# Kernel tuning notes

Measured on AMD Instinct MI355X. Metric: run time of the kernel, lower is better.

## Reference

```python
import jax, jax.numpy as jnp
import numpy as np

N, D, NUM_CLASSES = 8192, 256, 64
MARGIN_SAME = 0.9
MARGIN_DIFF = 0.5


def setup_inputs() -> dict:
    key = jax.random.key(0)
    k1, k2 = jax.random.split(key)
    inputs = jax.random.normal(k1, (N, D), dtype=jnp.float32)
    # contrastive losses with cosine-style margins expect unit-norm embeddings
    inputs = inputs / jnp.linalg.norm(inputs, axis=1, keepdims=True)
    targets = jax.random.randint(k2, (N,), 0, NUM_CLASSES, dtype=jnp.int64)
    return {"inputs": inputs, "targets": targets}


def reference(inputs, targets):
    n = inputs.shape[0]
    sim = jnp.matmul(inputs, inputs.T)  # [n, n] pairwise similarities

    same = targets[:, None] == targets[None, :]  # [n, n]
    pos_mask = same & (sim < 1.0)                # pos_pair_ selection per row
    neg_mask = ~same                             # neg_pair_ selection per row

    pos_active = pos_mask & (sim < MARGIN_SAME)  # contribute 1 - sim
    neg_active = neg_mask & (sim > MARGIN_DIFF)  # contribute sim

    # sum over all rows, divided by n (sort in the original is irrelevant to sums)
    loss = (jnp.sum(jnp.where(pos_active, 1.0 - sim, 0.0))
            + jnp.sum(jnp.where(neg_active, sim, 0.0))) / n

    prec = jnp.float32(0.0)  # original: c is never incremented

    # original reports means of the LAST row's pos_pair_ / neg_pair_
    last_sim = sim[n - 1]
    lp = pos_mask[n - 1]
    ln = neg_mask[n - 1]
    mean_pos_sim = jnp.sum(jnp.where(lp, last_sim, 0.0)) / jnp.maximum(
        jnp.sum(lp).astype(jnp.float32), 1.0)
    mean_neg_sim = jnp.sum(jnp.where(ln, last_sim, 0.0)) / jnp.maximum(
        jnp.sum(ln).astype(jnp.float32), 1.0)

    return (loss, prec, mean_pos_sim, mean_neg_sim)
```

## Files before the change

### kernel.cpp

```cpp
#include <hip/hip_runtime.h>
#include <hip/hip_bf16.h>

#define N_ 8192
#define D_ 256
#define BM 128
#define BK 32
#define NB (N_ / BM)
#define NT (NB * (NB + 1) / 2)
#define KSTEPS (D_ / BK)

typedef __bf16 bf16x8 __attribute__((ext_vector_type(8)));
typedef float f32x4 __attribute__((ext_vector_type(4)));

__global__ void cvt_kernel(const float4* __restrict__ in, ushort4* __restrict__ out, int n4,
                           double* __restrict__ accd) {
  int i = blockIdx.x * blockDim.x + threadIdx.x;
  if (blockIdx.x == 0 && threadIdx.x < 128) accd[threadIdx.x] = 0.0;
  if (i >= n4) return;
  float4 v = in[i];
  union { __hip_bfloat16 h[4]; ushort4 u; } t;
  t.h[0] = __float2bfloat16(v.x);
  t.h[1] = __float2bfloat16(v.y);
  t.h[2] = __float2bfloat16(v.z);
  t.h[3] = __float2bfloat16(v.w);
  out[i] = t.u;
}

__global__ __launch_bounds__(256, 4) void simloss_kernel(
    const __hip_bfloat16* __restrict__ Xb, const int* __restrict__ tg,
    double* __restrict__ accd) {
  __shared__ __align__(16) char lds[32768];

  const int t = blockIdx.x;
  int bi = (int)(((2.0f * NB + 1.0f) -
                  sqrtf((2.0f * NB + 1.0f) * (2.0f * NB + 1.0f) - 8.0f * (float)t)) * 0.5f);
  if (bi < 0) bi = 0;
  if (bi > NB - 1) bi = NB - 1;
  while (((bi + 1) * NB - ((bi + 1) * bi) / 2) <= t) ++bi;
  while ((bi * NB - (bi * (bi - 1)) / 2) > t) --bi;
  const int bj = bi + (t - (bi * NB - (bi * (bi - 1)) / 2));

  const int tid = threadIdx.x;
  const int lane = tid & 63, wv = tid >> 6;
  const int wr = wv >> 1, wc = wv & 1;
  const int rowA0 = bi * BM, rowB0 = bj * BM;

  const int c0 = (wv * 2 + 0) * 64 + lane;
  const int c1 = (wv * 2 + 1) * 64 + lane;
  const int r0 = c0 >> 2, s0 = (c0 & 3) ^ ((r0 >> 1) & 3);
  const int r1 = c1 >> 2, s1 = (c1 & 3) ^ ((r1 >> 1) & 3);
  const __hip_bfloat16* gA0 = Xb + (size_t)(rowA0 + r0) * D_ + s0 * 8;
  const __hip_bfloat16* gA1 = Xb + (size_t)(rowA0 + r1) * D_ + s1 * 8;
  const __hip_bfloat16* gB0 = Xb + (size_t)(rowB0 + r0) * D_ + s0 * 8;
  const __hip_bfloat16* gB1 = Xb + (size_t)(rowB0 + r1) * D_ + s1 * 8;
  char* lA0 = lds + c0 * 16;
  char* lA1 = lds + c1 * 16;
  char* lB0 = lds + 16384 + c0 * 16;
  char* lB1 = lds + 16384 + c1 * 16;

#define GLDS(g, l) \
  __builtin_amdgcn_global_load_lds((const __attribute__((address_space(1))) void*)(g), \
                                   (__attribute__((address_space(3))) void*)(l), 16, 0, 0)
#define STAGE(buf, kt)                       \
  do {                                       \
    GLDS(gA0 + (kt) * BK, lA0 + (buf) * 8192); \
    GLDS(gA1 + (kt) * BK, lA1 + (buf) * 8192); \
    GLDS(gB0 + (kt) * BK, lB0 + (buf) * 8192); \
    GLDS(gB1 + (kt) * BK, lB1 + (buf) * 8192); \
  } while (0)

  const int fr = lane & 15, sl = lane >> 4;
  const int rswz = sl ^ ((fr >> 1) & 3);
  const int aoff = (wr * 64 + fr) * 64 + rswz * 16;
  const int boff = (wc * 64 + fr) * 64 + rswz * 16;

  f32x4 acc[4][4] = {};

  STAGE(0, 0);
  __syncthreads();
#pragma unroll
  for (int kt = 0; kt < KSTEPS; ++kt) {
    const int cur = kt & 1;
    if (kt < KSTEPS - 1) STAGE(cur ^ 1, kt + 1);
    const char* Ab = lds + cur * 8192;
    const char* Bb = lds + 16384 + cur * 8192;
    bf16x8 af[4], bfr[4];
#pragma unroll
    for (int m = 0; m < 4; ++m) af[m] = *(const bf16x8*)(Ab + aoff + m * 1024);
#pragma unroll
    for (int n = 0; n < 4; ++n) bfr[n] = *(const bf16x8*)(Bb + boff + n * 1024);
#pragma unroll
    for (int m = 0; m < 4; ++m)
#pragma unroll
      for (int n = 0; n < 4; ++n)
        acc[m][n] = __builtin_amdgcn_mfma_f32_16x16x32_bf16(af[m], bfr[n], acc[m][n], 0, 0, 0);
    __syncthreads();
  }
#undef STAGE
#undef GLDS

  const int cRow = (lane >> 4) * 4, cCol = lane & 15;
  int tj[4], ti[4][4];
#pragma unroll
  for (int n = 0; n < 4; ++n) tj[n] = tg[rowB0 + wc * 64 + n * 16 + cCol];
#pragma unroll
  for (int m = 0; m < 4; ++m)
#pragma unroll
    for (int r = 0; r < 4; ++r) ti[m][r] = tg[rowA0 + wr * 64 + m * 16 + cRow + r];

  float pc = 0.f, ps = 0.f, ns = 0.f;
#pragma unroll
  for (int m = 0; m < 4; ++m)
#pragma unroll
    for (int n = 0; n < 4; ++n)
#pragma unroll
      for (int r = 0; r < 4; ++r) {
        float s = acc[m][n][r];
        bool same = (ti[m][r] == tj[n]);
        if (same & (s < 0.9f)) { pc += 1.0f; ps += s; }
        if ((!same) & (s > 0.5f)) { ns += s; }
      }

  if (bj == NB - 1 && wc == 1 && cCol == 15) {
    const int tlast = tj[3];
    float lps = 0.f, lns = 0.f, lpc = 0.f, lnc = 0.f;
#pragma unroll
    for (int m = 0; m < 4; ++m)
#pragma unroll
      for (int r = 0; r < 4; ++r) {
        float s = acc[m][3][r];
        bool same = (ti[m][r] == tlast);
        if (same && s < 1.0f) { lps += s; lpc += 1.f; }
        if (!same) { lns += s; lnc += 1.f; }
      }
    atomicAdd(&accd[96], (double)lps);
    atomicAdd(&accd[97], (double)lpc);
    atomicAdd(&accd[98], (double)lns);
    atomicAdd(&accd[99], (double)lnc);
  }

#pragma unroll
  for (int off = 32; off > 0; off >>= 1) {
    pc += __shfl_down(pc, off);
    ps += __shfl_down(ps, off);
    ns += __shfl_down(ns, off);
  }
  float* red = (float*)lds;
  if (lane == 0) { red[0 * 4 + wv] = pc; red[1 * 4 + wv] = ps; red[2 * 4 + wv] = ns; }
  __syncthreads();
  if (tid == 0) {
    double w = (bi == bj) ? 1.0 : 2.0;
    double* slot = accd + (blockIdx.x & 31) * 3;
    atomicAdd(&slot[0], w * (double)(red[0] + red[1] + red[2] + red[3]));
    atomicAdd(&slot[1], w * (double)(red[4] + red[5] + red[6] + red[7]));
    atomicAdd(&slot[2], w * (double)(red[8] + red[9] + red[10] + red[11]));
  }
}

__global__ void finalize_kernel(const double* __restrict__ accd, float* __restrict__ out) {
  double pc = 0.0, ps = 0.0, ns = 0.0;
#pragma unroll
  for (int i = 0; i < 32; ++i) {
    pc += accd[i * 3 + 0];
    ps += accd[i * 3 + 1];
    ns += accd[i * 3 + 2];
  }
  double loss = (pc - ps + ns) / (double)N_;
  out[0] = (float)loss;
  out[1] = 0.0f;
  out[2] = (float)(accd[96] / fmax(accd[97], 1.0));
  out[3] = (float)(accd[98] / fmax(accd[99], 1.0));
}

extern "C" void kernel_launch(void* const* d_in, const int* in_sizes, int n_in,
                              void* d_out, int out_size, void* d_ws, size_t ws_size,
                              hipStream_t stream) {
  const float* X = (const float*)d_in[0];
  const int* tg = (const int*)d_in[1];
  float* out = (float*)d_out;
  double* accd = (double*)d_ws;
  __hip_bfloat16* Xb = (__hip_bfloat16*)((char*)d_ws + 1024);

  int n4 = N_ * D_ / 4;
  cvt_kernel<<<(n4 + 255) / 256, 256, 0, stream>>>((const float4*)X, (ushort4*)Xb, n4, accd);

  simloss_kernel<<<NT, 256, 0, stream>>>(Xb, tg, accd);

  finalize_kernel<<<1, 1, 0, stream>>>(accd, out);
}
```

Before: 49.76 us.

## Load MFMA operands directly from global memory instead of LDS staging

Drops the double-buffered global-to-LDS staging and its per-step barriers. Each lane now reads its bf16x8 MFMA fragments straight from global memory, depending on L1/L2 cache for reuse across waves. This removes LDS traffic and synchronisation and frees LDS for occupancy, but it duplicates global loads across waves and loses the explicit prefetch overlap.

```diff
diff --git a/kernel.cpp b/kernel.cpp
--- a/kernel.cpp
+++ b/kernel.cpp
@@ -4,10 +4,9 @@
 #define N_ 8192
 #define D_ 256
 #define BM 128
-#define BK 32
 #define NB (N_ / BM)
 #define NT (NB * (NB + 1) / 2)
-#define KSTEPS (D_ / BK)
+#define KSTEPS (D_ / 32)
 
 typedef __bf16 bf16x8 __attribute__((ext_vector_type(8)));
 typedef float f32x4 __attribute__((ext_vector_type(4)));
@@ -29,8 +28,6 @@
 __global__ __launch_bounds__(256, 4) void simloss_kernel(
     const __hip_bfloat16* __restrict__ Xb, const int* __restrict__ tg,
     double* __restrict__ accd) {
-  __shared__ __align__(16) char lds[32768];
-
   const int t = blockIdx.x;
   int bi = (int)(((2.0f * NB + 1.0f) -
                   sqrtf((2.0f * NB + 1.0f) * (2.0f * NB + 1.0f) - 8.0f * (float)t)) * 0.5f);
@@ -45,61 +42,33 @@
   const int wr = wv >> 1, wc = wv & 1;
   const int rowA0 = bi * BM, rowB0 = bj * BM;
 
-  const int c0 = (wv * 2 + 0) * 64 + lane;
-  const int c1 = (wv * 2 + 1) * 64 + lane;
-  const int r0 = c0 >> 2, s0 = (c0 & 3) ^ ((r0 >> 1) & 3);
-  const int r1 = c1 >> 2, s1 = (c1 & 3) ^ ((r1 >> 1) & 3);
-  const __hip_bfloat16* gA0 = Xb + (size_t)(rowA0 + r0) * D_ + s0 * 8;
-  const __hip_bfloat16* gA1 = Xb + (size_t)(rowA0 + r1) * D_ + s1 * 8;
-  const __hip_bfloat16* gB0 = Xb + (size_t)(rowB0 + r0) * D_ + s0 * 8;
-  const __hip_bfloat16* gB1 = Xb + (size_t)(rowB0 + r1) * D_ + s1 * 8;
-  char* lA0 = lds + c0 * 16;
-  char* lA1 = lds + c1 * 16;
-  char* lB0 = lds + 16384 + c0 * 16;
-  char* lB1 = lds + 16384 + c1 * 16;
-
-#define GLDS(g, l) \
-  __builtin_amdgcn_global_load_lds((const __attribute__((address_space(1))) void*)(g), \
-                                   (__attribute__((address_space(3))) void*)(l), 16, 0, 0)
-#define STAGE(buf, kt)                       \
-  do {                                       \
-    GLDS(gA0 + (kt) * BK, lA0 + (buf) * 8192); \
-    GLDS(gA1 + (kt) * BK, lA1 + (buf) * 8192); \
-    GLDS(gB0 + (kt) * BK, lB0 + (buf) * 8192); \
-    GLDS(gB1 + (kt) * BK, lB1 + (buf) * 8192); \
-  } while (0)
-
   const int fr = lane & 15, sl = lane >> 4;
-  const int rswz = sl ^ ((fr >> 1) & 3);
-  const int aoff = (wr * 64 + fr) * 64 + rswz * 16;
-  const int boff = (wc * 64 + fr) * 64 + rswz * 16;
+  const __hip_bfloat16* pA[4];
+  const __hip_bfloat16* pB[4];
+#pragma unroll
+  for (int m = 0; m < 4; ++m)
+    pA[m] = Xb + (size_t)(rowA0 + wr * 64 + m * 16 + fr) * D_ + sl * 8;
+#pragma unroll
+  for (int n = 0; n < 4; ++n)
+    pB[n] = Xb + (size_t)(rowB0 + wc * 64 + n * 16 + fr) * D_ + sl * 8;
 
   f32x4 acc[4][4] = {};
 
-  STAGE(0, 0);
-  __syncthreads();
 #pragma unroll
   for (int kt = 0; kt < KSTEPS; ++kt) {
-    const int cur = kt & 1;
-    if (kt < KSTEPS - 1) STAGE(cur ^ 1, kt + 1);
-    const char* Ab = lds + cur * 8192;
-    const char* Bb = lds + 16384 + cur * 8192;
     bf16x8 af[4], bfr[4];
 #pragma unroll
-    for (int m = 0; m < 4; ++m) af[m] = *(const bf16x8*)(Ab + aoff + m * 1024);
+    for (int m = 0; m < 4; ++m) af[m] = *(const bf16x8*)(pA[m] + kt * 32);
 #pragma unroll
-    for (int n = 0; n < 4; ++n) bfr[n] = *(const bf16x8*)(Bb + boff + n * 1024);
+    for (int n = 0; n < 4; ++n) bfr[n] = *(const bf16x8*)(pB[n] + kt * 32);
 #pragma unroll
     for (int m = 0; m < 4; ++m)
 #pragma unroll
       for (int n = 0; n < 4; ++n)
         acc[m][n] = __builtin_amdgcn_mfma_f32_16x16x32_bf16(af[m], bfr[n], acc[m][n], 0, 0, 0);
-    __syncthreads();
   }
-#undef STAGE
-#undef GLDS
 
-  const int cRow = (lane >> 4) * 4, cCol = lane & 15;
+  const int cRow = sl * 4, cCol = fr;
   int tj[4], ti[4][4];
 #pragma unroll
   for (int n = 0; n < 4; ++n) tj[n] = tg[rowB0 + wc * 64 + n * 16 + cCol];
@@ -145,8 +114,8 @@
     ps += __shfl_down(ps, off);
     ns += __shfl_down(ns, off);
   }
-  float* red = (float*)lds;
-  if (lane == 0) { red[0 * 4 + wv] = pc; red[1 * 4 + wv] = ps; red[2 * 4 + wv] = ns; }
+  __shared__ float red[12];
+  if (lane == 0) { red[0 + wv] = pc; red[4 + wv] = ps; red[8 + wv] = ns; }
   __syncthreads();
   if (tid == 0) {
     double w = (bi == bj) ? 1.0 : 2.0;
```

Measured after the change: 93.21 us. +87.3%, slower.

## Triple-buffer LDS with explicit vmcnt waits and remap tile order

Applied to the files above, without the earlier changes.

Replaces the double-buffered K loop with a three-stage ring buffer. Loads for steps 0-2 are issued up front, and explicit s_waitcnt vmcnt counts plus raw barriers allow two global->LDS stages to stay in flight while MFMAs run. The block index is also permuted with a stride so neighbouring blocks map to tiles spread across the triangle, which likely changes L2 locality. Launch bounds drop to 3 blocks/CU to make room for the 48KB of LDS, trading occupancy for deeper prefetch. Correctness depends on the hand-counted vmcnt values matching the issued loads.

```diff
diff --git a/kernel.cpp b/kernel.cpp
--- a/kernel.cpp
+++ b/kernel.cpp
@@ -26,12 +26,14 @@
   out[i] = t.u;
 }
 
-__global__ __launch_bounds__(256, 4) void simloss_kernel(
+__global__ __launch_bounds__(256, 3) void simloss_kernel(
     const __hip_bfloat16* __restrict__ Xb, const int* __restrict__ tg,
     double* __restrict__ accd) {
-  __shared__ __align__(16) char lds[32768];
-
-  const int t = blockIdx.x;
+  __shared__ __align__(16) char lds[3 * 16384];
+
+  const int t0 = blockIdx.x;
+  const int t = (t0 & 7) * (NT / 8) + (t0 >> 3);
+
   int bi = (int)(((2.0f * NB + 1.0f) -
                   sqrtf((2.0f * NB + 1.0f) * (2.0f * NB + 1.0f) - 8.0f * (float)t)) * 0.5f);
   if (bi < 0) bi = 0;
@@ -53,20 +55,17 @@
   const __hip_bfloat16* gA1 = Xb + (size_t)(rowA0 + r1) * D_ + s1 * 8;
   const __hip_bfloat16* gB0 = Xb + (size_t)(rowB0 + r0) * D_ + s0 * 8;
   const __hip_bfloat16* gB1 = Xb + (size_t)(rowB0 + r1) * D_ + s1 * 8;
-  char* lA0 = lds + c0 * 16;
-  char* lA1 = lds + c1 * 16;
-  char* lB0 = lds + 16384 + c0 * 16;
-  char* lB1 = lds + 16384 + c1 * 16;
 
 #define GLDS(g, l) \
   __builtin_amdgcn_global_load_lds((const __attribute__((address_space(1))) void*)(g), \
                                    (__attribute__((address_space(3))) void*)(l), 16, 0, 0)
-#define STAGE(buf, kt)                       \
-  do {                                       \
-    GLDS(gA0 + (kt) * BK, lA0 + (buf) * 8192); \
-    GLDS(gA1 + (kt) * BK, lA1 + (buf) * 8192); \
-    GLDS(gB0 + (kt) * BK, lB0 + (buf) * 8192); \
-    GLDS(gB1 + (kt) * BK, lB1 + (buf) * 8192); \
+#define STAGE(buf, kt)                                    \
+  do {                                                    \
+    char* base = lds + (buf) * 16384;                     \
+    GLDS(gA0 + (kt) * BK, base + c0 * 16);                \
+    GLDS(gA1 + (kt) * BK, base + c1 * 16);                \
+    GLDS(gB0 + (kt) * BK, base + 8192 + c0 * 16);         \
+    GLDS(gB1 + (kt) * BK, base + 8192 + c1 * 16);         \
   } while (0)
 
   const int fr = lane & 15, sl = lane >> 4;
@@ -77,13 +76,21 @@
   f32x4 acc[4][4] = {};
 
   STAGE(0, 0);
-  __syncthreads();
+  STAGE(1, 1);
+  STAGE(2, 2);
+
 #pragma unroll
   for (int kt = 0; kt < KSTEPS; ++kt) {
-    const int cur = kt & 1;
-    if (kt < KSTEPS - 1) STAGE(cur ^ 1, kt + 1);
-    const char* Ab = lds + cur * 8192;
-    const char* Bb = lds + 16384 + cur * 8192;
+    if (kt < 6)
+      asm volatile("s_waitcnt vmcnt(8)" ::: "memory");
+    else if (kt == 6)
+      asm volatile("s_waitcnt vmcnt(4)" ::: "memory");
+    else
+      asm volatile("s_waitcnt vmcnt(0)" ::: "memory");
+    __builtin_amdgcn_s_barrier();
+
+    const char* Ab = lds + (kt % 3) * 16384;
+    const char* Bb = Ab + 8192;
     bf16x8 af[4], bfr[4];
 #pragma unroll
     for (int m = 0; m < 4; ++m) af[m] = *(const bf16x8*)(Ab + aoff + m * 1024);
@@ -94,12 +101,16 @@
 #pragma unroll
       for (int n = 0; n < 4; ++n)
         acc[m][n] = __builtin_amdgcn_mfma_f32_16x16x32_bf16(af[m], bfr[n], acc[m][n], 0, 0, 0);
-    __syncthreads();
+
+    asm volatile("s_waitcnt lgkmcnt(0)" ::: "memory");
+    __builtin_amdgcn_sched_barrier(0);
+    __builtin_amdgcn_s_barrier();
+    if (kt + 3 < KSTEPS) STAGE(kt % 3, kt + 3);
   }
 #undef STAGE
 #undef GLDS
 
-  const int cRow = (lane >> 4) * 4, cCol = lane & 15;
+  const int cRow = sl * 4, cCol = fr;
   int tj[4], ti[4][4];
 #pragma unroll
   for (int n = 0; n < 4; ++n) tj[n] = tg[rowB0 + wc * 64 + n * 16 + cCol];
@@ -146,7 +157,7 @@
     ns += __shfl_down(ns, off);
   }
   float* red = (float*)lds;
-  if (lane == 0) { red[0 * 4 + wv] = pc; red[1 * 4 + wv] = ps; red[2 * 4 + wv] = ns; }
+  if (lane == 0) { red[0 + wv] = pc; red[4 + wv] = ps; red[8 + wv] = ns; }
   __syncthreads();
   if (tid == 0) {
     double w = (bi == bj) ? 1.0 : 2.0;
```

Result: faster. 39.99 us (-19.6%).
